# Kernel optimization log

Measured on AMD Instinct MI355X. Metric: run time of the kernel, lower is better.

## Reference

```python
import jax, jax.numpy as jnp
import numpy as np

B, S, H, NH, SLOTS, SD = 4, 2048, 1024, 16, 16, 32
HD = H // NH  # head_dim = 64


def setup_inputs() -> dict:
    key = jax.random.key(0)
    ks = jax.random.split(key, 8)
    def w(k, shape, scale=0.02):
        return jax.random.normal(k, shape, jnp.float32) * scale
    return {
        "hidden_states": jax.random.normal(ks[0], (B, S, H), jnp.float32),
        "stack": jax.random.normal(ks[1], (B, S, NH, SLOTS, SD), jnp.float32),
        "mask": jnp.ones((B, S, NH, SLOTS), jnp.float32),
        "Wa": w(ks[2], (H, 3 * NH)), "ba": jnp.zeros((3 * NH,), jnp.float32),
        "Wd": w(ks[3], (HD, SD)), "bd": jnp.zeros((SD,), jnp.float32),
        "Wu": w(ks[4], (SD, HD)), "bu": jnp.zeros((HD,), jnp.float32),
        "Wg": w(ks[5], (SD, 1)), "bg": jnp.zeros((1,), jnp.float32),
        "res_weight": jnp.ones((1,), jnp.float32),
    }


def reference(hidden_states, stack, mask, Wa, ba, Wd, bd, Wu, bu, Wg, bg, res_weight):
    b, s, h = hidden_states.shape
    # action logits, scaled by sqrt(head_dim), softmax over {push,pop,noop}
    logits = (hidden_states @ Wa + ba) / jnp.sqrt(jnp.float32(HD))
    actions = jax.nn.softmax(logits.reshape(b, s, NH, 3), axis=-1)  # [B,S,NH,3]
    # per-head key values projected down to stack_dim
    k = hidden_states.reshape(b, s, NH, HD) @ Wd + bd  # [B,S,NH,SD]
    # soft push / pop / noop stack update (fused weighted sum; no [.,3,.] stack tensor)
    push_stack = jnp.concatenate([k[..., None, :], stack[..., :-1, :]], axis=3)
    pop_stack = jnp.concatenate([stack[..., 1:, :], jnp.zeros_like(stack[..., :1, :])], axis=3)
    push_mask = jnp.concatenate([jnp.ones_like(mask[..., :1]), mask[..., :-1]], axis=3)
    pop_mask = jnp.concatenate([mask[..., 1:], jnp.zeros_like(mask[..., :1])], axis=3)
    a_push = actions[..., 0]
    a_pop = actions[..., 1]
    a_noop = actions[..., 2]
    new_stack = (a_push[..., None, None] * push_stack
                 + a_pop[..., None, None] * pop_stack
                 + a_noop[..., None, None] * stack)  # [B,S,NH,SLOTS,SD]
    new_mask = (a_push[..., None] * push_mask
                + a_pop[..., None] * pop_mask
                + a_noop[..., None] * mask)  # [B,S,NH,SLOTS]
    # gated readout over stack slots
    gate_scores = (new_stack @ Wg)[..., 0] + bg[0]  # [B,S,NH,SLOTS]
    gate = jax.nn.softmax(gate_scores + (1.0 - new_mask) * -1e9, axis=-1)
    mem = jnp.sum(new_stack * gate[..., None], axis=3)  # [B,S,NH,SD]
    mem = mem @ Wu + bu  # [B,S,NH,HD]
    out = mem.reshape(b, s, h) * res_weight[0] + hidden_states
    return (out, new_stack, new_mask)
```

## Files before the change

kernel.cpp:

```cpp
#include <hip/hip_runtime.h>


constexpr int HDIM  = 1024;
constexpr int COLS  = 273;

constexpr long long OUT_STACK_OFF = 8388608LL;
constexpr long long OUT_MASK_OFF  = 75497472LL;

__global__ void transpose_wa(const float* __restrict__ Wa, float* __restrict__ WaT) {
    int o = blockIdx.x * 256 + threadIdx.x;
    if (o < 48 * 1024) {
        int j = o >> 10, i = o & 1023;
        WaT[o] = Wa[i * 48 + j];
    }
}

__global__ __launch_bounds__(256, 4)
void stack_fused(const float* __restrict__ hid,
                 const float* __restrict__ stack,
                 const float* __restrict__ mask,
                 const float* __restrict__ WaT,
                 const float* __restrict__ ba,
                 const float* __restrict__ Wd,
                 const float* __restrict__ bd,
                 const float* __restrict__ Wu,
                 const float* __restrict__ bu,
                 const float* __restrict__ Wg,
                 const float* __restrict__ bg,
                 const float* __restrict__ resw,
                 float* __restrict__ out)
{
    __shared__ float shT[32 * COLS];
    __shared__ float sh_logits[48];
    __shared__ float sh_mask[256];
    __shared__ float sh_mem[16 * 33];

    const int t   = threadIdx.x;
    const int tok = blockIdx.x;
    const float4* hid4 = (const float4*)(hid + (size_t)tok * HDIM);
    const float4* stk4 = (const float4*)(stack + (size_t)tok * 8192);

    if (t < 32) shT[t * COLS + 272] = 0.f;

    #pragma unroll
    for (int i = 0; i < 8; ++i) {
        float4 v = stk4[i * 256 + t];
        int e0  = (i * 256 + t) * 4;
        int row = e0 >> 5;
        int d0  = e0 & 31;
        int col = (row >> 4) * 17 + 1 + (row & 15);
        shT[(d0 + 0) * COLS + col] = v.x;
        shT[(d0 + 1) * COLS + col] = v.y;
        shT[(d0 + 2) * COLS + col] = v.z;
        shT[(d0 + 3) * COLS + col] = v.w;
    }
    sh_mask[t] = mask[(size_t)tok * 256 + t];

    const int wv = t >> 6, lane = t & 63;
    float4 hreg[4];
    #pragma unroll
    for (int m = 0; m < 4; ++m) hreg[m] = hid4[m * 64 + lane];
    const float4* waT4 = (const float4*)WaT;
    #pragma unroll
    for (int jj = 0; jj < 12; ++jj) {
        int j = wv * 12 + jj;
        float acc = 0.f;
        #pragma unroll
        for (int m = 0; m < 4; ++m) {
            float4 w = waT4[j * 256 + m * 64 + lane];
            acc += hreg[m].x * w.x + hreg[m].y * w.y + hreg[m].z * w.z + hreg[m].w * w.w;
        }
        #pragma unroll
        for (int off = 32; off >= 1; off >>= 1) acc += __shfl_xor(acc, off);
        if (lane == jj) sh_logits[j] = (acc + ba[j]) * 0.125f;
    }

    {
        int d = t & 31;
        int nh0 = t >> 5, nh1 = nh0 + 8;
        float acc0 = bd[d], acc1 = bd[d];
        #pragma unroll
        for (int ii = 0; ii < 16; ++ii) {
            float4 ha = hid4[nh0 * 16 + ii];
            float4 hb = hid4[nh1 * 16 + ii];
            float w0 = Wd[(4 * ii + 0) * 32 + d];
            float w1 = Wd[(4 * ii + 1) * 32 + d];
            float w2 = Wd[(4 * ii + 2) * 32 + d];
            float w3 = Wd[(4 * ii + 3) * 32 + d];
            acc0 += ha.x * w0 + ha.y * w1 + ha.z * w2 + ha.w * w3;
            acc1 += hb.x * w0 + hb.y * w1 + hb.z * w2 + hb.w * w3;
        }
        shT[d * COLS + nh0 * 17] = acc0;
        shT[d * COLS + nh1 * 17] = acc1;
    }
    __syncthreads();

    const int nh = t >> 4, slot = t & 15;
    float l0 = sh_logits[nh * 3 + 0];
    float l1 = sh_logits[nh * 3 + 1];
    float l2 = sh_logits[nh * 3 + 2];
    float mx = fmaxf(l0, fmaxf(l1, l2));
    float e0 = __expf(l0 - mx), e1 = __expf(l1 - mx), e2 = __expf(l2 - mx);
    float inv = 1.f / (e0 + e1 + e2);
    float a_push = e0 * inv, a_pop = e1 * inv, a_noop = e2 * inv;

    const int colC = nh * 17 + 1 + slot;
    const bool last = (slot == 15);
    float nr[32];
    float gs = 0.f;
    #pragma unroll
    for (int d = 0; d < 32; ++d) {
        float pv = shT[d * COLS + colC - 1];
        float cv = shT[d * COLS + colC];
        float nv = last ? 0.f : shT[d * COLS + colC + 1];
        float v  = a_push * pv + a_pop * nv + a_noop * cv;
        nr[d] = v;
        gs += v * Wg[d];
    }
    gs += bg[0];

    float pm = (slot == 0) ? 1.f : sh_mask[t - 1];
    float cm = sh_mask[t];
    float nm = last ? 0.f : sh_mask[t + 1];
    float nmask = a_push * pm + a_pop * nm + a_noop * cm;

    {
        float4* os4 = (float4*)(out + OUT_STACK_OFF + (size_t)tok * 8192 + t * 32);
        #pragma unroll
        for (int q = 0; q < 8; ++q)
            os4[q] = make_float4(nr[4*q], nr[4*q+1], nr[4*q+2], nr[4*q+3]);
        out[OUT_MASK_OFF + (size_t)tok * 256 + t] = nmask;
    }

    float gb = gs + (1.f - nmask) * -1e9f;
    float gm = gb;
    #pragma unroll
    for (int off = 8; off >= 1; off >>= 1) gm = fmaxf(gm, __shfl_xor(gm, off));
    float ge = __expf(gb - gm);
    float gsum = ge;
    #pragma unroll
    for (int off = 8; off >= 1; off >>= 1) gsum += __shfl_xor(gsum, off);
    float gate = ge / gsum;

    __syncthreads();
    #pragma unroll
    for (int d = 0; d < 32; ++d) shT[d * COLS + colC] = gate * nr[d];
    __syncthreads();

    #pragma unroll
    for (int r = 0; r < 2; ++r) {
        int o = t + r * 256;
        int onh = o >> 5, od = o & 31;
        const float* p = &shT[od * COLS + onh * 17 + 1];
        float s = 0.f;
        #pragma unroll
        for (int sl = 0; sl < 16; ++sl) s += p[sl];
        sh_mem[onh * 33 + od] = s;
    }
    __syncthreads();

    {
        int o0  = t * 4;
        int onh = o0 >> 6;
        int hd0 = o0 & 63;
        float4 acc = *(const float4*)(bu + hd0);
        const float* memrow = &sh_mem[onh * 33];
        const float4* Wu4 = (const float4*)Wu;
        #pragma unroll
        for (int d = 0; d < 32; ++d) {
            float mv = memrow[d];
            float4 w = Wu4[d * 16 + (hd0 >> 2)];
            acc.x += mv * w.x; acc.y += mv * w.y; acc.z += mv * w.z; acc.w += mv * w.w;
        }
        float rw = resw[0];
        float4 hres = hid4[t];
        acc.x = acc.x * rw + hres.x;
        acc.y = acc.y * rw + hres.y;
        acc.z = acc.z * rw + hres.z;
        acc.w = acc.w * rw + hres.w;
        *(float4*)(out + (size_t)tok * HDIM + o0) = acc;
    }
}

extern "C" void kernel_launch(void* const* d_in, const int* in_sizes, int n_in,
                              void* d_out, int out_size, void* d_ws, size_t ws_size,
                              hipStream_t stream) {
    const float* hid  = (const float*)d_in[0];
    const float* stk  = (const float*)d_in[1];
    const float* msk  = (const float*)d_in[2];
    const float* Wa   = (const float*)d_in[3];
    const float* ba   = (const float*)d_in[4];
    const float* Wd   = (const float*)d_in[5];
    const float* bd   = (const float*)d_in[6];
    const float* Wu   = (const float*)d_in[7];
    const float* bu   = (const float*)d_in[8];
    const float* Wg   = (const float*)d_in[9];
    const float* bg   = (const float*)d_in[10];
    const float* rw   = (const float*)d_in[11];
    float* out = (float*)d_out;
    float* waT = (float*)d_ws;

    transpose_wa<<<192, 256, 0, stream>>>(Wa, waT);
    stack_fused<<<8192, 256, 0, stream>>>(hid, stk, msk, waT, ba, Wd, bd, Wu, bu, Wg, bg, rw, out);
}
```

Before: 670.4 us.

## Split into projection kernel and per-head wavefront stack kernel using shuffles

Replaces the per-token fused block with two kernels. The first computes action logits and key projections four tokens per block, so weight loads are reused, and stashes them in the output stack buffer. The second assigns one wavefront per (token, head) and does the slot shift, gate softmax and readout with cross-lane shuffles instead of a transposed shared-memory tile. This removes the large LDS staging and most block barriers, at the cost of an extra launch and a global round trip through the stash region, which the second kernel then overwrites.

```diff
diff --git a/kernel.cpp b/kernel.cpp
--- a/kernel.cpp
+++ b/kernel.cpp
@@ -1,8 +1,5 @@
 #include <hip/hip_runtime.h>
 
-
-constexpr int HDIM  = 1024;
-constexpr int COLS  = 273;
 
 constexpr long long OUT_STACK_OFF = 8388608LL;
 constexpr long long OUT_MASK_OFF  = 75497472LL;
@@ -15,171 +12,211 @@
     }
 }
 
-__global__ __launch_bounds__(256, 4)
-void stack_fused(const float* __restrict__ hid,
-                 const float* __restrict__ stack,
-                 const float* __restrict__ mask,
+__device__ __forceinline__ float dot4(float4 a, float4 b) {
+    return a.x * b.x + a.y * b.y + a.z * b.z + a.w * b.w;
+}
+
+__device__ __forceinline__ float4 shfl4(float4 v, int src) {
+    return make_float4(__shfl(v.x, src), __shfl(v.y, src),
+                       __shfl(v.z, src), __shfl(v.w, src));
+}
+
+__device__ __forceinline__ float4 sel4(bool c, float4 a, float4 b) {
+    return make_float4(c ? a.x : b.x, c ? a.y : b.y, c ? a.z : b.z, c ? a.w : b.w);
+}
+
+__global__ __launch_bounds__(256)
+void proj_kernel(const float* __restrict__ hid,
                  const float* __restrict__ WaT,
                  const float* __restrict__ ba,
                  const float* __restrict__ Wd,
                  const float* __restrict__ bd,
-                 const float* __restrict__ Wu,
-                 const float* __restrict__ bu,
-                 const float* __restrict__ Wg,
-                 const float* __restrict__ bg,
-                 const float* __restrict__ resw,
                  float* __restrict__ out)
 {
-    __shared__ float shT[32 * COLS];
-    __shared__ float sh_logits[48];
-    __shared__ float sh_mask[256];
-    __shared__ float sh_mem[16 * 33];
-
-    const int t   = threadIdx.x;
-    const int tok = blockIdx.x;
-    const float4* hid4 = (const float4*)(hid + (size_t)tok * HDIM);
-    const float4* stk4 = (const float4*)(stack + (size_t)tok * 8192);
-
-    if (t < 32) shT[t * COLS + 272] = 0.f;
-
-    #pragma unroll
-    for (int i = 0; i < 8; ++i) {
-        float4 v = stk4[i * 256 + t];
-        int e0  = (i * 256 + t) * 4;
-        int row = e0 >> 5;
-        int d0  = e0 & 31;
-        int col = (row >> 4) * 17 + 1 + (row & 15);
-        shT[(d0 + 0) * COLS + col] = v.x;
-        shT[(d0 + 1) * COLS + col] = v.y;
-        shT[(d0 + 2) * COLS + col] = v.z;
-        shT[(d0 + 3) * COLS + col] = v.w;
-    }
-    sh_mask[t] = mask[(size_t)tok * 256 + t];
-
+    const int t = threadIdx.x;
     const int wv = t >> 6, lane = t & 63;
-    float4 hreg[4];
-    #pragma unroll
-    for (int m = 0; m < 4; ++m) hreg[m] = hid4[m * 64 + lane];
+    const int tok0 = blockIdx.x * 4;
+    float* stash = out + OUT_STACK_OFF;
+    const float4* hid4 = (const float4*)hid + (size_t)tok0 * 256;
+
+    float4 hreg[4][4];
+    #pragma unroll
+    for (int tt = 0; tt < 4; ++tt)
+        #pragma unroll
+        for (int m = 0; m < 4; ++m)
+            hreg[tt][m] = hid4[tt * 256 + m * 64 + lane];
+
     const float4* waT4 = (const float4*)WaT;
     #pragma unroll
     for (int jj = 0; jj < 12; ++jj) {
         int j = wv * 12 + jj;
-        float acc = 0.f;
+        float a0 = 0.f, a1 = 0.f, a2 = 0.f, a3 = 0.f;
         #pragma unroll
         for (int m = 0; m < 4; ++m) {
             float4 w = waT4[j * 256 + m * 64 + lane];
-            acc += hreg[m].x * w.x + hreg[m].y * w.y + hreg[m].z * w.z + hreg[m].w * w.w;
-        }
-        #pragma unroll
-        for (int off = 32; off >= 1; off >>= 1) acc += __shfl_xor(acc, off);
-        if (lane == jj) sh_logits[j] = (acc + ba[j]) * 0.125f;
-    }
-
-    {
-        int d = t & 31;
-        int nh0 = t >> 5, nh1 = nh0 + 8;
-        float acc0 = bd[d], acc1 = bd[d];
-        #pragma unroll
-        for (int ii = 0; ii < 16; ++ii) {
-            float4 ha = hid4[nh0 * 16 + ii];
-            float4 hb = hid4[nh1 * 16 + ii];
-            float w0 = Wd[(4 * ii + 0) * 32 + d];
-            float w1 = Wd[(4 * ii + 1) * 32 + d];
-            float w2 = Wd[(4 * ii + 2) * 32 + d];
-            float w3 = Wd[(4 * ii + 3) * 32 + d];
-            acc0 += ha.x * w0 + ha.y * w1 + ha.z * w2 + ha.w * w3;
-            acc1 += hb.x * w0 + hb.y * w1 + hb.z * w2 + hb.w * w3;
-        }
-        shT[d * COLS + nh0 * 17] = acc0;
-        shT[d * COLS + nh1 * 17] = acc1;
-    }
+            a0 += dot4(hreg[0][m], w);
+            a1 += dot4(hreg[1][m], w);
+            a2 += dot4(hreg[2][m], w);
+            a3 += dot4(hreg[3][m], w);
+        }
+        #pragma unroll
+        for (int off = 1; off <= 32; off <<= 1) {
+            a0 += __shfl_xor(a0, off);
+            a1 += __shfl_xor(a1, off);
+            a2 += __shfl_xor(a2, off);
+            a3 += __shfl_xor(a3, off);
+        }
+        if ((lane & 15) == jj) {
+            int tt = lane >> 4;
+            float v = (tt == 0) ? a0 : (tt == 1) ? a1 : (tt == 2) ? a2 : a3;
+            int nh = wv * 4 + jj / 3, a = jj - 3 * (jj / 3);
+            stash[(size_t)(tok0 + tt) * 8192 + nh * 512 + 32 + a] = (v + ba[j]) * 0.125f;
+        }
+    }
+
+    const int d = t & 31, nhg = t >> 5;
+    float acc0[4], acc1[4];
+    float bdv = bd[d];
+    #pragma unroll
+    for (int tt = 0; tt < 4; ++tt) { acc0[tt] = bdv; acc1[tt] = bdv; }
+    #pragma unroll
+    for (int ii = 0; ii < 16; ++ii) {
+        float w0 = Wd[(4 * ii + 0) * 32 + d];
+        float w1 = Wd[(4 * ii + 1) * 32 + d];
+        float w2 = Wd[(4 * ii + 2) * 32 + d];
+        float w3 = Wd[(4 * ii + 3) * 32 + d];
+        #pragma unroll
+        for (int tt = 0; tt < 4; ++tt) {
+            float4 ha = hid4[tt * 256 + nhg * 16 + ii];
+            float4 hb = hid4[tt * 256 + (nhg + 8) * 16 + ii];
+            acc0[tt] += ha.x * w0 + ha.y * w1 + ha.z * w2 + ha.w * w3;
+            acc1[tt] += hb.x * w0 + hb.y * w1 + hb.z * w2 + hb.w * w3;
+        }
+    }
+    #pragma unroll
+    for (int tt = 0; tt < 4; ++tt) {
+        stash[(size_t)(tok0 + tt) * 8192 + nhg * 512 + d] = acc0[tt];
+        stash[(size_t)(tok0 + tt) * 8192 + (nhg + 8) * 512 + d] = acc1[tt];
+    }
+}
+
+__global__ __launch_bounds__(256, 4)
+void stack_main(const float* __restrict__ stack,
+                const float* __restrict__ mask,
+                const float* __restrict__ hid,
+                const float* __restrict__ Wg,
+                const float* __restrict__ bgp,
+                const float* __restrict__ Wu,
+                const float* __restrict__ bu,
+                const float* __restrict__ resw,
+                float* __restrict__ out)
+{
+    __shared__ __align__(16) float sh_mem[4][32];
+    const int t = threadIdx.x, wv = t >> 6, l = t & 63;
+    const int wid = blockIdx.x * 4 + wv;
+    const int tok = wid >> 4, nh = wid & 15;
+
+    const float4* stk4 = (const float4*)stack + (size_t)tok * 2048 + nh * 128;
+    float* ostack = out + OUT_STACK_OFF + (size_t)tok * 8192 + nh * 512;
+    const float4* stash4 = (const float4*)ostack;
+
+    float4 A  = stk4[l];
+    float4 Bv = stk4[64 + l];
+    float4 kv = stash4[l & 7];
+    float4 lg = stash4[8];
+    const float* mrow_g = mask + (size_t)tok * 256 + nh * 16;
+    float mA = mrow_g[l >> 3];
+    float mB = mrow_g[8 + (l >> 3)];
+    float4 wg = *(const float4*)(Wg + (l & 7) * 4);
+
+    float mx = fmaxf(lg.x, fmaxf(lg.y, lg.z));
+    float e0 = __expf(lg.x - mx), e1 = __expf(lg.y - mx), e2 = __expf(lg.z - mx);
+    float ainv = 1.f / (e0 + e1 + e2);
+    float ap = e0 * ainv, apop = e1 * ainv, an = e2 * ainv;
+
+    float4 Am  = shfl4(A,  l - 8);
+    float4 Apl = shfl4(A,  l + 8);
+    float4 BfA = shfl4(A,  l + 56);
+    float4 AfB = shfl4(Bv, l - 56);
+    float4 Bm  = shfl4(Bv, l - 8);
+    float4 Bp  = shfl4(Bv, l + 8);
+    float sAm = __shfl(mA, l - 8), sAp = __shfl(mA, l + 8), sA56 = __shfl(mA, l + 56);
+    float sBm = __shfl(mB, l - 8), sBp = __shfl(mB, l + 8), sB56 = __shfl(mB, l - 56);
+
+    const bool lo = (l < 8), hi = (l >= 56);
+    float4 prevA = sel4(lo, kv, Am);
+    float4 nextA = sel4(hi, AfB, Apl);
+    float4 prevB = sel4(lo, BfA, Bm);
+    float4 nextB = sel4(hi, make_float4(0.f, 0.f, 0.f, 0.f), Bp);
+    float pmA = lo ? 1.f : sAm;
+    float nmA = hi ? sB56 : sAp;
+    float pmB = lo ? sA56 : sBm;
+    float nmB = hi ? 0.f : sBp;
+
+    float4 nA, nB;
+    nA.x = ap * prevA.x + apop * nextA.x + an * A.x;
+    nA.y = ap * prevA.y + apop * nextA.y + an * A.y;
+    nA.z = ap * prevA.z + apop * nextA.z + an * A.z;
+    nA.w = ap * prevA.w + apop * nextA.w + an * A.w;
+    nB.x = ap * prevB.x + apop * nextB.x + an * Bv.x;
+    nB.y = ap * prevB.y + apop * nextB.y + an * Bv.y;
+    nB.z = ap * prevB.z + apop * nextB.z + an * Bv.z;
+    nB.w = ap * prevB.w + apop * nextB.w + an * Bv.w;
+    float nmaskA = ap * pmA + apop * nmA + an * mA;
+    float nmaskB = ap * pmB + apop * nmB + an * mB;
+
+    float4* ost4 = (float4*)ostack;
+    ost4[l] = nA;
+    ost4[64 + l] = nB;
+    if ((l & 7) == 0) {
+        float* om = out + OUT_MASK_OFF + (size_t)tok * 256 + nh * 16;
+        om[l >> 3] = nmaskA;
+        om[8 + (l >> 3)] = nmaskB;
+    }
+
+    float gA = dot4(nA, wg);
+    float gB = dot4(nB, wg);
+    #pragma unroll
+    for (int off = 1; off <= 4; off <<= 1) {
+        gA += __shfl_xor(gA, off);
+        gB += __shfl_xor(gB, off);
+    }
+    float bgv = bgp[0];
+    gA += bgv + (1.f - nmaskA) * -1e9f;
+    gB += bgv + (1.f - nmaskB) * -1e9f;
+
+    float gm = fmaxf(gA, gB);
+    #pragma unroll
+    for (int off = 8; off <= 32; off <<= 1) gm = fmaxf(gm, __shfl_xor(gm, off));
+    float eA = __expf(gA - gm), eB = __expf(gB - gm);
+    float es = eA + eB;
+    #pragma unroll
+    for (int off = 8; off <= 32; off <<= 1) es += __shfl_xor(es, off);
+    float ginv = 1.f / es;
+    float gateA = eA * ginv, gateB = eB * ginv;
+
+    float4 sv;
+    sv.x = gateA * nA.x + gateB * nB.x;
+    sv.y = gateA * nA.y + gateB * nB.y;
+    sv.z = gateA * nA.z + gateB * nB.z;
+    sv.w = gateA * nA.w + gateB * nB.w;
+    #pragma unroll
+    for (int off = 8; off <= 32; off <<= 1) {
+        sv.x += __shfl_xor(sv.x, off);
+        sv.y += __shfl_xor(sv.y, off);
+        sv.z += __shfl_xor(sv.z, off);
+        sv.w += __shfl_xor(sv.w, off);
+    }
+    if (l < 8) *(float4*)&sh_mem[wv][l * 4] = sv;
     __syncthreads();
 
-    const int nh = t >> 4, slot = t & 15;
-    float l0 = sh_logits[nh * 3 + 0];
-    float l1 = sh_logits[nh * 3 + 1];
-    float l2 = sh_logits[nh * 3 + 2];
-    float mx = fmaxf(l0, fmaxf(l1, l2));
-    float e0 = __expf(l0 - mx), e1 = __expf(l1 - mx), e2 = __expf(l2 - mx);
-    float inv = 1.f / (e0 + e1 + e2);
-    float a_push = e0 * inv, a_pop = e1 * inv, a_noop = e2 * inv;
-
-    const int colC = nh * 17 + 1 + slot;
-    const bool last = (slot == 15);
-    float nr[32];
-    float gs = 0.f;
-    #pragma unroll
-    for (int d = 0; d < 32; ++d) {
-        float pv = shT[d * COLS + colC - 1];
-        float cv = shT[d * COLS + colC];
-        float nv = last ? 0.f : shT[d * COLS + colC + 1];
-        float v  = a_push * pv + a_pop * nv + a_noop * cv;
-        nr[d] = v;
-        gs += v * Wg[d];
-    }
-    gs += bg[0];
-
-    float pm = (slot == 0) ? 1.f : sh_mask[t - 1];
-    float cm = sh_mask[t];
-    float nm = last ? 0.f : sh_mask[t + 1];
-    float nmask = a_push * pm + a_pop * nm + a_noop * cm;
-
-    {
-        float4* os4 = (float4*)(out + OUT_STACK_OFF + (size_t)tok * 8192 + t * 32);
-        #pragma unroll
-        for (int q = 0; q < 8; ++q)
-            os4[q] = make_float4(nr[4*q], nr[4*q+1], nr[4*q+2], nr[4*q+3]);
-        out[OUT_MASK_OFF + (size_t)tok * 256 + t] = nmask;
-    }
-
-    float gb = gs + (1.f - nmask) * -1e9f;
-    float gm = gb;
-    #pragma unroll
-    for (int off = 8; off >= 1; off >>= 1) gm = fmaxf(gm, __shfl_xor(gm, off));
-    float ge = __expf(gb - gm);
-    float gsum = ge;
-    #pragma unroll
-    for (int off = 8; off >= 1; off >>= 1) gsum += __shfl_xor(gsum, off);
-    float gate = ge / gsum;
-
-    __syncthreads();
-    #pragma unroll
-    for (int d = 0; d < 32; ++d) shT[d * COLS + colC] = gate * nr[d];
-    __syncthreads();
-
-    #pragma unroll
-    for (int r = 0; r < 2; ++r) {
-        int o = t + r * 256;
-        int onh = o >> 5, od = o & 31;
-        const float* p = &shT[od * COLS + onh * 17 + 1];
-        float s = 0.f;
-        #pragma unroll
-        for (int sl = 0; sl < 16; ++sl) s += p[sl];
-        sh_mem[onh * 33 + od] = s;
-    }
-    __syncthreads();
-
-    {
-        int o0  = t * 4;
-        int onh = o0 >> 6;
-        int hd0 = o0 & 63;
-        float4 acc = *(const float4*)(bu + hd0);
-        const float* memrow = &sh_mem[onh * 33];
-        const float4* Wu4 = (const float4*)Wu;
-        #pragma unroll
-        for (int d = 0; d < 32; ++d) {
-            float mv = memrow[d];
-            float4 w = Wu4[d * 16 + (hd0 >> 2)];
-            acc.x += mv * w.x; acc.y += mv * w.y; acc.z += mv * w.z; acc.w += mv * w.w;
-        }
-        float rw = resw[0];
-        float4 hres = hid4[t];
-        acc.x = acc.x * rw + hres.x;
-        acc.y = acc.y * rw + hres.y;
-        acc.z = acc.z * rw + hres.z;
-        acc.w = acc.w * rw + hres.w;
-        *(float4*)(out + (size_t)tok * HDIM + o0) = acc;
-    }
+    float acc = bu[l];
+    const float* mrow = sh_mem[wv];
+    #pragma unroll
+    for (int dd = 0; dd < 32; ++dd)
+        acc += mrow[dd] * Wu[dd * 64 + l];
+    size_t oidx = (size_t)tok * 1024 + nh * 64 + l;
+    out[oidx] = acc * resw[0] + hid[oidx];
 }
 
 extern "C" void kernel_launch(void* const* d_in, const int* in_sizes, int n_in,
@@ -201,5 +238,6 @@
     float* waT = (float*)d_ws;
 
     transpose_wa<<<192, 256, 0, stream>>>(Wa, waT);
-    stack_fused<<<8192, 256, 0, stream>>>(hid, stk, msk, waT, ba, Wd, bd, Wu, bu, Wg, bg, rw, out);
-}
+    proj_kernel<<<2048, 256, 0, stream>>>(hid, waT, ba, Wd, bd, out);
+    stack_main<<<32768, 256, 0, stream>>>(stk, msk, hid, Wg, bg, Wu, bu, rw, out);
+}
```

After: 596.7 us. -11.0%, faster.
